# Performance work log

Hardware: AMD Instinct MI355X
Metric: run time of the kernel (lower is better)

Reference implementation:

```python
import jax, jax.numpy as jnp
import numpy as np

N_NODES = 512
HEADS = 4
CO = 64        # per-head out channels (PyG GATConv out_channels)
NEG_SLOPE = 0.2  # PyG GATConv default negative_slope


def setup_inputs() -> dict:
    key = jax.random.key(0)
    k0, k1, k2, k3, k4 = jax.random.split(key, 5)
    B, C, T, N = 8, 64, 12, N_NODES
    E = 8192
    x = jax.random.normal(k0, (B, C, T, N), dtype=jnp.float32)
    edge_index = jax.random.randint(k1, (2, E), 0, N, dtype=jnp.int32)
    # learned params of GATConv(in=64, out=64, heads=4, concat=False)
    W = jax.random.normal(k2, (C, HEADS * CO), dtype=jnp.float32) / np.sqrt(C).astype(np.float32)
    att_src = jax.random.normal(k3, (HEADS, CO), dtype=jnp.float32) * 0.1
    att_dst = jax.random.normal(k4, (HEADS, CO), dtype=jnp.float32) * 0.1
    bias = jnp.zeros((CO,), dtype=jnp.float32)
    return {"x": x, "edge_index": edge_index, "W": W,
            "att_src": att_src, "att_dst": att_dst, "bias": bias}


def reference(x, edge_index, W, att_src, att_dst, bias):
    # x: [B, C, T, N] -> batch of G = B*T graphs, all sharing edge_index.
    B, C, T, N = x.shape
    H, Co = att_src.shape
    G = B * T
    xg = x.transpose(0, 2, 3, 1).reshape(G, N, C)              # [G,N,C]
    h = (xg @ W).reshape(G, N, H, Co)                          # [G,N,H,Co]
    a_src = jnp.einsum('gnhc,hc->gnh', h, att_src)             # [G,N,H]
    a_dst = jnp.einsum('gnhc,hc->gnh', h, att_dst)             # [G,N,H]
    # add self loops (PyG GATConv default)
    loops = jnp.arange(N, dtype=edge_index.dtype)
    src = jnp.concatenate([edge_index[0], loops])              # [E']
    dst = jnp.concatenate([edge_index[1], loops])              # [E']
    # attention logits per edge, leading edge axis for segment ops
    logits = jax.nn.leaky_relu(a_src[:, src] + a_dst[:, dst], NEG_SLOPE)  # [G,E',H]
    logits = logits.transpose(1, 0, 2)                         # [E',G,H]
    m = jax.ops.segment_max(logits, dst, num_segments=N)       # [N,G,H]
    e = jnp.exp(logits - m[dst])
    s = jax.ops.segment_sum(e, dst, num_segments=N)            # [N,G,H]
    alpha = e / s[dst]                                         # [E',G,H]  (dropout off: eval)
    msg = alpha[..., None] * h[:, src].transpose(1, 0, 2, 3)   # [E',G,H,Co]
    out = jax.ops.segment_sum(msg, dst, num_segments=N)        # [N,G,H,Co]
    out = out.mean(axis=2) + bias                              # [N,G,Co]  concat=False -> head mean
    out = out.transpose(1, 0, 2).reshape(B, T, N, Co)          # [B,T,N,Co]
    return out.transpose(0, 3, 1, 2)                           # [B,Co,T,N]
```

## Files before the change

### kernel.cpp

```cpp
#include <hip/hip_runtime.h>

#define B_  8
#define C_  64
#define T_  12
#define N_  512
#define E_  8192
#define H_  4
#define CO_ 64
#define G_  (B_ * T_)
#define EP_ (E_ + N_)
#define MAXDEG 128

typedef __bf16 bf16x8 __attribute__((ext_vector_type(8)));
typedef unsigned short usx8 __attribute__((ext_vector_type(8)));
typedef float  f32x4  __attribute__((ext_vector_type(4)));

static __device__ __forceinline__ unsigned short f2bf(float f) {
    unsigned int u = __float_as_uint(f);
    return (unsigned short)((u + 0x7fffu + ((u >> 16) & 1u)) >> 16);
}

__global__ __launch_bounds__(512) void k_prep(
    const float* __restrict__ x, const int* __restrict__ ei,
    const float* __restrict__ W,
    const float* __restrict__ att_src, const float* __restrict__ att_dst,
    float* __restrict__ xt, float* __restrict__ as_t, float* __restrict__ ad_t,
    int* __restrict__ off, int* __restrict__ srclist,
    unsigned short* __restrict__ Wfrag)
{
    int tid = threadIdx.x;

    if (blockIdx.x == 384) {
        __shared__ int lcnt[512];
        __shared__ int lscan[512];

        for (int idx = tid; idx < 64 * 256; idx += 512) {
            int c  = idx >> 8, r = idx & 255;
            int hh = r >> 6,  co = r & 63;
            int k  = hh * 64 + c;
            int ks = k >> 5, kq = (k >> 3) & 3, j = k & 7;
            int nt = co >> 4, l = kq * 16 + (co & 15);
            Wfrag[(size_t)((ks * 4 + nt) * 64 + l) * 8 + j] = f2bf(W[idx]);
        }

        lcnt[tid] = 1;
        __syncthreads();
        for (int e = tid; e < E_; e += 512)
            atomicAdd(&lcnt[ei[E_ + e]], 1);
        __syncthreads();
        int v = lcnt[tid];
        lscan[tid] = v;
        __syncthreads();
        for (int d = 1; d < 512; d <<= 1) {
            int val = (tid >= d) ? lscan[tid - d] : 0;
            __syncthreads();
            lscan[tid] += val;
            __syncthreads();
        }
        int excl = lscan[tid] - v;
        off[tid] = excl;
        if (tid == 511) off[512] = lscan[511];
        lcnt[tid] = excl;
        __syncthreads();
        for (int e = tid; e < EP_; e += 512) {
            int d, s;
            if (e < E_) { d = ei[E_ + e]; s = ei[e]; }
            else        { d = e - E_;     s = d; }
            int pos = atomicAdd(&lcnt[d], 1);
            srclist[pos] = s;
        }
        return;
    }

    __shared__ float xs[2][64][65];
    __shared__ float Wls[64][4], Wld[64][4];

    if (tid < 256) {
        int c = tid & 63, hh = tid >> 6;
        float s1 = 0.f, s2 = 0.f;
        for (int co = 0; co < 64; ++co) {
            float w = W[c * 256 + hh * 64 + co];
            s1 += w * att_src[hh * 64 + co];
            s2 += w * att_dst[hh * 64 + co];
        }
        Wls[c][hh] = s1;
        Wld[c][hh] = s2;
    }

    int half = tid >> 8;
    int t256 = tid & 255;
    int lane = t256 & 63, q = t256 >> 6;
    int tile_id = blockIdx.x * 2 + half;
    int g  = tile_id >> 3, tl = tile_id & 7;
    int b  = g / T_, t = g - b * T_;
    int n0 = tl * 64;

    #pragma unroll
    for (int i = 0; i < 16; ++i) {
        int c = q + i * 4;
        xs[half][c][lane] = x[((size_t)(b * C_ + c) * T_ + t) * N_ + n0 + lane];
    }
    __syncthreads();

    float s1 = 0.f, s2 = 0.f;
    for (int c = 0; c < 64; ++c) {
        float v = xs[half][c][lane];
        s1 += v * Wls[c][q];
        s2 += v * Wld[c][q];
    }
    int n = n0 + lane;
    as_t[((size_t)q * N_ + n) * G_ + g] = s1;
    ad_t[((size_t)q * N_ + n) * G_ + g] = s2;

    #pragma unroll
    for (int i = 0; i < 16; ++i) {
        int nl = q + i * 4;
        xt[((size_t)(g * N_ + n0 + nl)) * 64 + lane] = xs[half][lane][nl];
    }
}

__global__ __launch_bounds__(256) void k_aggr(
    const float* __restrict__ xt, const float* __restrict__ as_t,
    const float* __restrict__ ad_t,
    const int* __restrict__ off, const int* __restrict__ srclist,
    unsigned short* __restrict__ zb)
{
    __shared__ float wbuf[MAXDEG][4][4];
    __shared__ int   ssrc[MAXDEG];
    int tid  = threadIdx.x;
    int wave = tid >> 6, lane = tid & 63;
    int xcd  = blockIdx.x & 7;
    int slot = blockIdx.x >> 3;
    int n    = slot & 511;
    int gq   = slot >> 9;
    int g0   = xcd * 12 + gq * 4;
    int o0   = off[n], deg = off[n + 1] - o0;

    if (tid < deg) ssrc[tid] = srclist[o0 + tid];

    int sub = tid & 15, p = tid >> 4;
    int hh = sub >> 2, gl = sub & 3;
    int gg = g0 + gl;
    float adv = ad_t[((size_t)hh * N_ + n) * G_ + gg];
    for (int e = p; e < deg; e += 16) {
        int s = srclist[o0 + e];
        float v = as_t[((size_t)hh * N_ + s) * G_ + gg] + adv;
        v = v > 0.f ? v : 0.2f * v;
        wbuf[e][gl][hh] = __expf(v);
    }
    __syncthreads();

    int g = g0 + wave;
    const float* xg = xt + (size_t)g * N_ * 64 + lane;
    float z0 = 0.f, z1 = 0.f, z2 = 0.f, z3 = 0.f;
    float s0 = 0.f, s1 = 0.f, s2 = 0.f, s3 = 0.f;
    int e = 0;
    for (; e + 8 <= deg; e += 8) {
        float xv[8];
        #pragma unroll
        for (int u = 0; u < 8; ++u) xv[u] = xg[(size_t)ssrc[e + u] * 64];
        #pragma unroll
        for (int u = 0; u < 8; ++u) {
            float4 w = *reinterpret_cast<const float4*>(&wbuf[e + u][wave][0]);
            z0 += w.x * xv[u];  s0 += w.x;
            z1 += w.y * xv[u];  s1 += w.y;
            z2 += w.z * xv[u];  s2 += w.z;
            z3 += w.w * xv[u];  s3 += w.w;
        }
    }
    for (; e < deg; ++e) {
        float xv = xg[(size_t)ssrc[e] * 64];
        float4 w = *reinterpret_cast<const float4*>(&wbuf[e][wave][0]);
        z0 += w.x * xv;  s0 += w.x;
        z1 += w.y * xv;  s1 += w.y;
        z2 += w.z * xv;  s2 += w.z;
        z3 += w.w * xv;  s3 += w.w;
    }
    size_t base = ((size_t)g * N_ + n) * 256 + lane;
    zb[base +   0] = f2bf(z0 / s0);
    zb[base +  64] = f2bf(z1 / s1);
    zb[base + 128] = f2bf(z2 / s2);
    zb[base + 192] = f2bf(z3 / s3);
}

__global__ __launch_bounds__(256) void k_out(
    const unsigned short* __restrict__ zb, const unsigned short* __restrict__ Wfrag,
    const float* __restrict__ bias, float* __restrict__ out)
{
    __shared__ char lds[32768];
    unsigned short (*Bfr)[4][64][8] = (unsigned short (*)[4][64][8])lds;
    float (*tl)[65] = (float (*)[65])lds;

    int bid  = blockIdx.x;
    int xcd  = bid & 7;
    int r    = bid >> 3;
    int g    = xcd * 12 + (r >> 3);
    int tile = r & 7;
    int b    = g / T_, t = g - b * T_;
    int n0   = tile * 64;
    int tid  = threadIdx.x;

    {
        const float4* src = reinterpret_cast<const float4*>(Wfrag);
        float4* dst = reinterpret_cast<float4*>(&Bfr[0][0][0][0]);
        #pragma unroll
        for (int it = 0; it < 8; ++it)
            dst[tid + it * 256] = src[tid + it * 256];
    }
    __syncthreads();

    int i = tid >> 6, l = tid & 63;
    int m = l & 15, quad = l >> 4;
    const unsigned short* zrow = zb + ((size_t)(g * N_) + n0 + i * 16 + m) * 256 + quad * 8;

    f32x4 acc[4];
    #pragma unroll
    for (int nt = 0; nt < 4; ++nt) acc[nt] = (f32x4){0.f, 0.f, 0.f, 0.f};

    #pragma unroll
    for (int ks = 0; ks < 8; ++ks) {
        usx8 ua = *reinterpret_cast<const usx8*>(zrow + ks * 32);
        bf16x8 a = __builtin_bit_cast(bf16x8, ua);
        #pragma unroll
        for (int nt = 0; nt < 4; ++nt) {
            bf16x8 bw = *reinterpret_cast<bf16x8*>(&Bfr[ks][nt][l][0]);
            acc[nt] = __builtin_amdgcn_mfma_f32_16x16x32_bf16(a, bw, acc[nt], 0, 0, 0);
        }
    }
    __syncthreads();

    #pragma unroll
    for (int nt = 0; nt < 4; ++nt) {
        int co = nt * 16 + m;
        float bv = bias[co];
        #pragma unroll
        for (int rr = 0; rr < 4; ++rr) {
            int row = i * 16 + quad * 4 + rr;
            tl[row][co] = 0.25f * acc[nt][rr] + bv;
        }
    }
    __syncthreads();

    #pragma unroll
    for (int it = 0; it < 16; ++it) {
        int c = i + it * 4;
        out[((size_t)(b * CO_ + c) * T_ + t) * N_ + n0 + l] = tl[l][c];
    }
}

extern "C" void kernel_launch(void* const* d_in, const int* in_sizes, int n_in,
                              void* d_out, int out_size, void* d_ws, size_t ws_size,
                              hipStream_t stream) {
    const float* x       = (const float*)d_in[0];
    const int*   ei      = (const int*)  d_in[1];
    const float* W       = (const float*)d_in[2];
    const float* att_src = (const float*)d_in[3];
    const float* att_dst = (const float*)d_in[4];
    const float* bias    = (const float*)d_in[5];
    float* out = (float*)d_out;

    char* p = (char*)d_ws;
    float* xt      = (float*)p;  p += (size_t)G_ * N_ * C_ * sizeof(float);
    unsigned short* zb = (unsigned short*)p; p += (size_t)G_ * N_ * 256 * sizeof(unsigned short);
    float* as_t    = (float*)p;  p += (size_t)H_ * N_ * G_ * sizeof(float);
    float* ad_t    = (float*)p;  p += (size_t)H_ * N_ * G_ * sizeof(float);
    unsigned short* Wfrag = (unsigned short*)p; p += 64 * 256 * sizeof(unsigned short);
    int* off       = (int*)p;    p += 516 * sizeof(int);
    int* srclist   = (int*)p;    p += EP_ * sizeof(int);

    k_prep  <<<385,      512, 0, stream>>>(x, ei, W, att_src, att_dst,
                                           xt, as_t, ad_t, off, srclist, Wfrag);
    k_aggr  <<<8 * 1536, 256, 0, stream>>>(xt, as_t, ad_t, off, srclist, zb);
    k_out   <<<G_ * 8,   256, 0, stream>>>(zb, Wfrag, bias, out);
}
```

Before: 131.4 us.

## Relayout attention scores node-major, split prep blocks, aggregate two nodes per block

Attention source/destination scores move from a head-major [H,N,G] layout to [G,N,H], and are staged through shared memory so the writes are contiguous. k_prep now uses 256-thread blocks, one tile each, with a vectorized W·att precompute and a two-elements-per-thread scan. k_aggr handles two destination nodes per block, halving the grid and amortizing the block setup. The risk is less parallelism in the aggregation kernel and serialized per-node loops within a block.

```diff
diff --git a/kernel.cpp b/kernel.cpp
--- a/kernel.cpp
+++ b/kernel.cpp
@@ -20,21 +20,21 @@
     return (unsigned short)((u + 0x7fffu + ((u >> 16) & 1u)) >> 16);
 }
 
-__global__ __launch_bounds__(512) void k_prep(
+__global__ __launch_bounds__(256) void k_prep(
     const float* __restrict__ x, const int* __restrict__ ei,
     const float* __restrict__ W,
     const float* __restrict__ att_src, const float* __restrict__ att_dst,
-    float* __restrict__ xt, float* __restrict__ as_t, float* __restrict__ ad_t,
+    float* __restrict__ xt, float* __restrict__ as_, float* __restrict__ ad_,
     int* __restrict__ off, int* __restrict__ srclist,
     unsigned short* __restrict__ Wfrag)
 {
     int tid = threadIdx.x;
 
-    if (blockIdx.x == 384) {
+    if (blockIdx.x == 768) {
         __shared__ int lcnt[512];
-        __shared__ int lscan[512];
-
-        for (int idx = tid; idx < 64 * 256; idx += 512) {
+        __shared__ int lsum[256];
+
+        for (int idx = tid; idx < 64 * 256; idx += 256) {
             int c  = idx >> 8, r = idx & 255;
             int hh = r >> 6,  co = r & 63;
             int k  = hh * 64 + c;
@@ -43,26 +43,29 @@
             Wfrag[(size_t)((ks * 4 + nt) * 64 + l) * 8 + j] = f2bf(W[idx]);
         }
 
-        lcnt[tid] = 1;
-        __syncthreads();
-        for (int e = tid; e < E_; e += 512)
+        lcnt[tid] = 1; lcnt[tid + 256] = 1;
+        __syncthreads();
+        for (int e = tid; e < E_; e += 256)
             atomicAdd(&lcnt[ei[E_ + e]], 1);
         __syncthreads();
-        int v = lcnt[tid];
-        lscan[tid] = v;
-        __syncthreads();
-        for (int d = 1; d < 512; d <<= 1) {
-            int val = (tid >= d) ? lscan[tid - d] : 0;
+        int v0 = lcnt[2 * tid], v1 = lcnt[2 * tid + 1];
+        lsum[tid] = v0 + v1;
+        __syncthreads();
+        for (int d = 1; d < 256; d <<= 1) {
+            int val = (tid >= d) ? lsum[tid - d] : 0;
             __syncthreads();
-            lscan[tid] += val;
+            lsum[tid] += val;
             __syncthreads();
         }
-        int excl = lscan[tid] - v;
-        off[tid] = excl;
-        if (tid == 511) off[512] = lscan[511];
-        lcnt[tid] = excl;
-        __syncthreads();
-        for (int e = tid; e < EP_; e += 512) {
+        int incl = lsum[tid];
+        int e0 = incl - v0 - v1;
+        off[2 * tid]     = e0;
+        off[2 * tid + 1] = e0 + v0;
+        if (tid == 255) off[512] = incl;
+        lcnt[2 * tid] = e0;
+        lcnt[2 * tid + 1] = e0 + v0;
+        __syncthreads();
+        for (int e = tid; e < EP_; e += 256) {
             int d, s;
             if (e < E_) { d = ei[E_ + e]; s = ei[e]; }
             else        { d = e - E_;     s = d; }
@@ -72,25 +75,29 @@
         return;
     }
 
-    __shared__ float xs[2][64][65];
+    __shared__ float xs[64][65];
     __shared__ float Wls[64][4], Wld[64][4];
-
-    if (tid < 256) {
-        int c = tid & 63, hh = tid >> 6;
+    __shared__ float sa[64][5], sd[64][5];
+
+    int lane = tid & 63, q = tid >> 6;
+
+    {
+        int c = lane, hh = q;
         float s1 = 0.f, s2 = 0.f;
-        for (int co = 0; co < 64; ++co) {
-            float w = W[c * 256 + hh * 64 + co];
-            s1 += w * att_src[hh * 64 + co];
-            s2 += w * att_dst[hh * 64 + co];
+        const float4* w4 = reinterpret_cast<const float4*>(W + c * 256 + hh * 64);
+        const float4* a1 = reinterpret_cast<const float4*>(att_src + hh * 64);
+        const float4* a2 = reinterpret_cast<const float4*>(att_dst + hh * 64);
+        #pragma unroll
+        for (int j = 0; j < 16; ++j) {
+            float4 w = w4[j], u = a1[j], v = a2[j];
+            s1 += w.x * u.x + w.y * u.y + w.z * u.z + w.w * u.w;
+            s2 += w.x * v.x + w.y * v.y + w.z * v.z + w.w * v.w;
         }
         Wls[c][hh] = s1;
         Wld[c][hh] = s2;
     }
 
-    int half = tid >> 8;
-    int t256 = tid & 255;
-    int lane = t256 & 63, q = t256 >> 6;
-    int tile_id = blockIdx.x * 2 + half;
+    int tile_id = blockIdx.x;
     int g  = tile_id >> 3, tl = tile_id & 7;
     int b  = g / T_, t = g - b * T_;
     int n0 = tl * 64;
@@ -98,89 +105,104 @@
     #pragma unroll
     for (int i = 0; i < 16; ++i) {
         int c = q + i * 4;
-        xs[half][c][lane] = x[((size_t)(b * C_ + c) * T_ + t) * N_ + n0 + lane];
+        xs[c][lane] = x[((size_t)(b * C_ + c) * T_ + t) * N_ + n0 + lane];
     }
     __syncthreads();
 
     float s1 = 0.f, s2 = 0.f;
     for (int c = 0; c < 64; ++c) {
-        float v = xs[half][c][lane];
+        float v = xs[c][lane];
         s1 += v * Wls[c][q];
         s2 += v * Wld[c][q];
     }
-    int n = n0 + lane;
-    as_t[((size_t)q * N_ + n) * G_ + g] = s1;
-    ad_t[((size_t)q * N_ + n) * G_ + g] = s2;
+    sa[lane][q] = s1;
+    sd[lane][q] = s2;
 
     #pragma unroll
     for (int i = 0; i < 16; ++i) {
         int nl = q + i * 4;
-        xt[((size_t)(g * N_ + n0 + nl)) * 64 + lane] = xs[half][lane][nl];
-    }
+        xt[((size_t)(g * N_ + n0 + nl)) * 64 + lane] = xs[lane][nl];
+    }
+    __syncthreads();
+
+    int nl = tid >> 2, hh = tid & 3;
+    as_[((size_t)(g * N_ + n0 + nl)) * 4 + hh] = sa[nl][hh];
+    ad_[((size_t)(g * N_ + n0 + nl)) * 4 + hh] = sd[nl][hh];
 }
 
 __global__ __launch_bounds__(256) void k_aggr(
-    const float* __restrict__ xt, const float* __restrict__ as_t,
-    const float* __restrict__ ad_t,
+    const float* __restrict__ xt, const float* __restrict__ as_,
+    const float* __restrict__ ad_,
     const int* __restrict__ off, const int* __restrict__ srclist,
     unsigned short* __restrict__ zb)
 {
-    __shared__ float wbuf[MAXDEG][4][4];
-    __shared__ int   ssrc[MAXDEG];
+    __shared__ float wbuf[2][MAXDEG][4][4];
+    __shared__ int   ssrc[2][MAXDEG];
     int tid  = threadIdx.x;
     int wave = tid >> 6, lane = tid & 63;
     int xcd  = blockIdx.x & 7;
     int slot = blockIdx.x >> 3;
-    int n    = slot & 511;
-    int gq   = slot >> 9;
+    int np   = slot & 255;
+    int gq   = slot >> 8;
     int g0   = xcd * 12 + gq * 4;
-    int o0   = off[n], deg = off[n + 1] - o0;
-
-    if (tid < deg) ssrc[tid] = srclist[o0 + tid];
+    int n0   = np * 2;
+    int o_a  = off[n0], o_b = off[n0 + 1], o_c = off[n0 + 2];
+    int dg[2] = {o_b - o_a, o_c - o_b};
+    int ob[2] = {o_a, o_b};
+
+    if (tid < dg[0]) ssrc[0][tid] = srclist[o_a + tid];
+    if (tid < dg[1]) ssrc[1][tid] = srclist[o_b + tid];
 
     int sub = tid & 15, p = tid >> 4;
-    int hh = sub >> 2, gl = sub & 3;
+    int hh = sub & 3, gl = sub >> 2;
     int gg = g0 + gl;
-    float adv = ad_t[((size_t)hh * N_ + n) * G_ + gg];
-    for (int e = p; e < deg; e += 16) {
-        int s = srclist[o0 + e];
-        float v = as_t[((size_t)hh * N_ + s) * G_ + gg] + adv;
-        v = v > 0.f ? v : 0.2f * v;
-        wbuf[e][gl][hh] = __expf(v);
+    #pragma unroll
+    for (int u = 0; u < 2; ++u) {
+        float adv = ad_[((size_t)(gg * N_ + n0 + u)) * 4 + hh];
+        for (int e = p; e < dg[u]; e += 16) {
+            int s = srclist[ob[u] + e];
+            float v = as_[((size_t)(gg * N_ + s)) * 4 + hh] + adv;
+            v = v > 0.f ? v : 0.2f * v;
+            wbuf[u][e][gl][hh] = __expf(v);
+        }
     }
     __syncthreads();
 
     int g = g0 + wave;
     const float* xg = xt + (size_t)g * N_ * 64 + lane;
-    float z0 = 0.f, z1 = 0.f, z2 = 0.f, z3 = 0.f;
-    float s0 = 0.f, s1 = 0.f, s2 = 0.f, s3 = 0.f;
-    int e = 0;
-    for (; e + 8 <= deg; e += 8) {
-        float xv[8];
-        #pragma unroll
-        for (int u = 0; u < 8; ++u) xv[u] = xg[(size_t)ssrc[e + u] * 64];
-        #pragma unroll
-        for (int u = 0; u < 8; ++u) {
-            float4 w = *reinterpret_cast<const float4*>(&wbuf[e + u][wave][0]);
-            z0 += w.x * xv[u];  s0 += w.x;
-            z1 += w.y * xv[u];  s1 += w.y;
-            z2 += w.z * xv[u];  s2 += w.z;
-            z3 += w.w * xv[u];  s3 += w.w;
-        }
-    }
-    for (; e < deg; ++e) {
-        float xv = xg[(size_t)ssrc[e] * 64];
-        float4 w = *reinterpret_cast<const float4*>(&wbuf[e][wave][0]);
-        z0 += w.x * xv;  s0 += w.x;
-        z1 += w.y * xv;  s1 += w.y;
-        z2 += w.z * xv;  s2 += w.z;
-        z3 += w.w * xv;  s3 += w.w;
-    }
-    size_t base = ((size_t)g * N_ + n) * 256 + lane;
-    zb[base +   0] = f2bf(z0 / s0);
-    zb[base +  64] = f2bf(z1 / s1);
-    zb[base + 128] = f2bf(z2 / s2);
-    zb[base + 192] = f2bf(z3 / s3);
+    #pragma unroll
+    for (int u = 0; u < 2; ++u) {
+        float z0 = 0.f, z1 = 0.f, z2 = 0.f, z3 = 0.f;
+        float s0 = 0.f, s1 = 0.f, s2 = 0.f, s3 = 0.f;
+        int deg = dg[u];
+        int e = 0;
+        for (; e + 8 <= deg; e += 8) {
+            float xv[8];
+            #pragma unroll
+            for (int j = 0; j < 8; ++j) xv[j] = xg[(size_t)ssrc[u][e + j] * 64];
+            #pragma unroll
+            for (int j = 0; j < 8; ++j) {
+                float4 w = *reinterpret_cast<const float4*>(&wbuf[u][e + j][wave][0]);
+                z0 += w.x * xv[j];  s0 += w.x;
+                z1 += w.y * xv[j];  s1 += w.y;
+                z2 += w.z * xv[j];  s2 += w.z;
+                z3 += w.w * xv[j];  s3 += w.w;
+            }
+        }
+        for (; e < deg; ++e) {
+            float xv = xg[(size_t)ssrc[u][e] * 64];
+            float4 w = *reinterpret_cast<const float4*>(&wbuf[u][e][wave][0]);
+            z0 += w.x * xv;  s0 += w.x;
+            z1 += w.y * xv;  s1 += w.y;
+            z2 += w.z * xv;  s2 += w.z;
+            z3 += w.w * xv;  s3 += w.w;
+        }
+        size_t base = ((size_t)g * N_ + n0 + u) * 256 + lane;
+        zb[base +   0] = f2bf(z0 / s0);
+        zb[base +  64] = f2bf(z1 / s1);
+        zb[base + 128] = f2bf(z2 / s2);
+        zb[base + 192] = f2bf(z3 / s3);
+    }
 }
 
 __global__ __launch_bounds__(256) void k_out(
@@ -262,14 +284,14 @@
     char* p = (char*)d_ws;
     float* xt      = (float*)p;  p += (size_t)G_ * N_ * C_ * sizeof(float);
     unsigned short* zb = (unsigned short*)p; p += (size_t)G_ * N_ * 256 * sizeof(unsigned short);
-    float* as_t    = (float*)p;  p += (size_t)H_ * N_ * G_ * sizeof(float);
-    float* ad_t    = (float*)p;  p += (size_t)H_ * N_ * G_ * sizeof(float);
+    float* as_     = (float*)p;  p += (size_t)G_ * N_ * H_ * sizeof(float);
+    float* ad_     = (float*)p;  p += (size_t)G_ * N_ * H_ * sizeof(float);
     unsigned short* Wfrag = (unsigned short*)p; p += 64 * 256 * sizeof(unsigned short);
     int* off       = (int*)p;    p += 516 * sizeof(int);
     int* srclist   = (int*)p;    p += EP_ * sizeof(int);
 
-    k_prep  <<<385,      512, 0, stream>>>(x, ei, W, att_src, att_dst,
-                                           xt, as_t, ad_t, off, srclist, Wfrag);
-    k_aggr  <<<8 * 1536, 256, 0, stream>>>(xt, as_t, ad_t, off, srclist, zb);
+    k_prep  <<<769,      256, 0, stream>>>(x, ei, W, att_src, att_dst,
+                                           xt, as_, ad_, off, srclist, Wfrag);
+    k_aggr  <<<8 * 768,  256, 0, stream>>>(xt, as_, ad_, off, srclist, zb);
     k_out   <<<G_ * 8,   256, 0, stream>>>(zb, Wfrag, bias, out);
 }
```

Result: slower. 145.8 us (+11.0%).
